# Optimization experiments

Measured on AMD Instinct MI355X. Metric: run time of the kernel, lower is better.

Reference implementation:

```python
import jax, jax.numpy as jnp
import numpy as np

B, S, H, NH = 8, 1042, 768, 12
HD = H // NH            # 64
P = 1024                # patch tokens (32x32 grid); RoPE applied to last P tokens
MLP = 2048              # int(768 * 8/3)
EPS = 1e-6


def _rope_tables():
    # mirrors precompute_rope_freqs_2d(HD, P): inside, dim = HD//2 = 32
    dim = HD // 2
    t = int(P ** 0.5)  # 32
    freqs = 1.0 / (10000.0 ** (np.arange(0, dim, 2, dtype=np.float32) / dim))  # (16,)
    pos = np.arange(t, dtype=np.float32)
    fh = pos[:, None] * freqs[None, :]                       # (t,16)
    f = np.concatenate([np.tile(fh[:, None, :], (1, t, 1)),
                        np.tile(fh[None, :, :], (t, 1, 1))], axis=-1)  # (t,t,32)
    f = f.reshape(P, dim)                                    # (1024,32)
    return jnp.asarray(np.cos(f)), jnp.asarray(np.sin(f))


def setup_inputs() -> dict:
    key = jax.random.key(0)
    ks = jax.random.split(key, 20)
    r = lambda k, sh, sc: (jax.random.normal(k, sh, jnp.float32) * sc)
    cos, sin = _rope_tables()
    return {
        "x": jax.random.normal(ks[0], (B, S, H), jnp.float32),
        "rope_cos": cos, "rope_sin": sin,
        "Wq": r(ks[1], (H, H), 0.02), "Wk": r(ks[2], (H, H), 0.02),
        "Wv": r(ks[3], (H, H), 0.02), "Wo": r(ks[4], (H, H), 0.02),
        "q_norm_w": jnp.ones((HD,), jnp.float32),
        "k_norm_w": jnp.ones((HD,), jnp.float32),
        "gate_W": r(ks[5], (H, NH), 0.02),
        "gate_b": jnp.full((NH,), 4.0, jnp.float32),
        "norm1_w": jnp.ones((H,), jnp.float32),
        "norm2_w": jnp.ones((H,), jnp.float32),
        "W_gate": r(ks[6], (H, MLP), 0.02),
        "W_up": r(ks[7], (H, MLP), 0.02),
        "W_down": r(ks[8], (MLP, H), 0.02),
        "attn_scale": r(ks[9], (H,), 0.1),   # zero-init in module; randn for nontrivial grads
        "mlp_scale": r(ks[10], (H,), 0.1),
    }


def _rmsnorm(x, w):
    return x * jax.lax.rsqrt(jnp.mean(x * x, axis=-1, keepdims=True) + EPS) * w


def _apply_rope(x, cos, sin):
    # x: (B,S,NH,HD); rotate only the last P (patch) tokens, consecutive-pair complex rotation
    xp = x[:, -P:].reshape(B, P, NH, HD // 2, 2)
    x0, x1 = xp[..., 0], xp[..., 1]
    c = cos[None, :, None, :]
    s = sin[None, :, None, :]
    rot = jnp.stack([x0 * c - x1 * s, x0 * s + x1 * c], axis=-1).reshape(B, P, NH, HD)
    return jnp.concatenate([x[:, :-P], rot], axis=1)


def reference(x, rope_cos, rope_sin, Wq, Wk, Wv, Wo, q_norm_w, k_norm_w,
              gate_W, gate_b, norm1_w, norm2_w, W_gate, W_up, W_down,
              attn_scale, mlp_scale):
    # --- attention branch (QwenGatedRoPEAttention) ---
    h = _rmsnorm(x, norm1_w)
    q = (h @ Wq).reshape(B, S, NH, HD)
    k = (h @ Wk).reshape(B, S, NH, HD)
    v = (h @ Wv).reshape(B, S, NH, HD)
    q = _rmsnorm(q, q_norm_w)
    k = _rmsnorm(k, k_norm_w)
    q = _apply_rope(q, rope_cos, rope_sin)
    k = _apply_rope(k, rope_cos, rope_sin)
    q = q / jnp.sqrt(jnp.asarray(HD, jnp.float32))
    scores = jnp.einsum('bqhd,bkhd->bhqk', q, k)          # (B,NH,S,S)
    probs = jax.nn.softmax(scores.astype(jnp.float32), axis=-1)
    attn = jnp.einsum('bhqk,bkhd->bqhd', probs, v)        # (B,S,NH,HD)
    gate = jax.nn.sigmoid((h @ gate_W)[..., None] + gate_b[None, None, :, None])
    attn = (attn * gate).reshape(B, S, H)
    x = x + (attn @ Wo) * attn_scale
    # --- SwiGLU MLP branch ---
    h2 = _rmsnorm(x, norm2_w)
    mlp = (jax.nn.silu(h2 @ W_gate) * (h2 @ W_up)) @ W_down
    x = x + mlp * mlp_scale
    return x
```

## Files before the change

kernel.cpp:

```cpp
#include <hip/hip_runtime.h>
#include <hip/hip_bf16.h>
#include <stdint.h>

#define B_   8
#define S_   1042
#define H_   768
#define NH_  12
#define HD_  64
#define MLP_ 2048
#define T_   (B_*S_)
#define MP_  8448
#define SP_  1088
#define EPS_ 1e-6f

typedef __attribute__((ext_vector_type(8))) short bf16x8v;
typedef __attribute__((ext_vector_type(4))) float f32x4;
typedef __hip_bfloat16 bf16;

typedef __attribute__((address_space(1))) const void gas_void;
typedef __attribute__((address_space(3))) void las_void;

__device__ inline void gload_lds16(const void* g, void* l) {
  __builtin_amdgcn_global_load_lds((gas_void*)g, (las_void*)l, 16, 0, 0);
}

#define BARRIER asm volatile("s_barrier" ::: "memory")
#define VMCNT4  asm volatile("s_waitcnt vmcnt(4)" ::: "memory")

__global__ __launch_bounds__(256) void wcvt_t(const float* __restrict__ W, bf16* __restrict__ o,
                                              int K, int N) {
  __shared__ float tile[32][33];
  int kt = blockIdx.x, nt = blockIdx.y;
  int t = threadIdx.x;
  int r = t >> 5, c = t & 31;
#pragma unroll
  for (int i = 0; i < 4; i++)
    tile[i * 8 + r][c] = W[(long)(kt * 32 + i * 8 + r) * N + nt * 32 + c];
  __syncthreads();
#pragma unroll
  for (int i = 0; i < 4; i++)
    o[(long)(nt * 32 + i * 8 + r) * K + kt * 32 + c] = __float2bfloat16(tile[c][i * 8 + r]);
}

__global__ __launch_bounds__(256) void wcvt_gu(const float* __restrict__ Wg,
                                               const float* __restrict__ Wu,
                                               bf16* __restrict__ o) {
  __shared__ float tile[32][33];
  int kt = blockIdx.x, nt = blockIdx.y;
  int t = threadIdx.x;
  int r = t >> 5, c = t & 31;
  const float* src = (c < 16) ? Wg : Wu;
  int col = nt * 16 + (c & 15);
#pragma unroll
  for (int i = 0; i < 4; i++)
    tile[i * 8 + r][c] = src[(long)(kt * 32 + i * 8 + r) * MLP_ + col];
  __syncthreads();
#pragma unroll
  for (int i = 0; i < 4; i++)
    o[(long)(nt * 32 + i * 8 + r) * 768 + kt * 32 + c] = __float2bfloat16(tile[c][i * 8 + r]);
}

__global__ __launch_bounds__(256) void rmsnorm_k(const float* __restrict__ x,
                                                 const float* __restrict__ w,
                                                 bf16* __restrict__ o, int Mreal) {
  int row = blockIdx.x;
  bf16* orow = o + (long)row * H_;
  int t = threadIdx.x;
  if (row >= Mreal) {
    for (int i = t; i < H_; i += 256) orow[i] = __float2bfloat16(0.f);
    return;
  }
  const float* xr = x + (long)row * H_;
  float v0 = xr[t], v1 = xr[t + 256], v2 = xr[t + 512];
  float s = v0 * v0 + v1 * v1 + v2 * v2;
  for (int off = 32; off; off >>= 1) s += __shfl_down(s, off);
  __shared__ float red[4];
  if ((t & 63) == 0) red[t >> 6] = s;
  __syncthreads();
  float tot = red[0] + red[1] + red[2] + red[3];
  float inv = rsqrtf(tot * (1.f / H_) + EPS_);
  orow[t]       = __float2bfloat16(v0 * inv * w[t]);
  orow[t + 256] = __float2bfloat16(v1 * inv * w[t + 256]);
  orow[t + 512] = __float2bfloat16(v2 * inv * w[t + 512]);
}

template <int EPI>
__global__ __launch_bounds__(512) void gemm256(
    const bf16* __restrict__ A, const bf16* __restrict__ Bt, void* __restrict__ Out,
    int N, int nbn) {
  __shared__ __align__(16) bf16 lds[2][4][128 * 64];
  int tid = threadIdx.x;
  int lane = tid & 63, wid = tid >> 6;
  int wr = wid >> 2, wc = wid & 3;
  int lr = lane & 15, lg = lane >> 4;

  int nwg = gridDim.x;
  int bid = blockIdx.x;
  int q = nwg >> 3, r8 = nwg & 7;
  int xcd = bid & 7, idx = bid >> 3;
  int wg = (xcd < r8 ? xcd * (q + 1) : r8 * (q + 1) + (xcd - r8) * q) + idx;
  int bm = wg / nbn, bn = wg - bm * nbn;

  int chunk_row = tid >> 3;
  int cc = (tid & 7) ^ (chunk_row & 7);
  const bf16* aSrc = A + ((long)bm * 256 + chunk_row) * 768 + cc * 8;
  const bf16* bSrc = Bt + ((long)bn * 256 + chunk_row) * 768 + cc * 8;

  auto stA = [&](int buf, int half, int kt) {
    bf16* d = &lds[buf][half][tid * 8];
    const bf16* s = aSrc + (long)half * 128 * 768 + kt * 64;
    gload_lds16(s, d);
    gload_lds16(s + 64 * 768, d + 512 * 8);
  };
  auto stB = [&](int buf, int half, int kt) {
    bf16* d = &lds[buf][2 + half][tid * 8];
    const bf16* s = bSrc + (long)half * 128 * 768 + kt * 64;
    gload_lds16(s, d);
    gload_lds16(s + 64 * 768, d + 512 * 8);
  };
  auto ldA = [&](int buf, int mi, int ks) -> bf16x8v {
    int row = mi * 16 + lr;
    int c = (ks * 4 + lg) ^ (row & 7);
    return *(const bf16x8v*)&lds[buf][wr][row * 64 + c * 8];
  };
  auto ldB = [&](int buf, int ni, int ks) -> bf16x8v {
    int row = (wc & 1) * 64 + ni * 16 + lr;
    int c = (ks * 4 + lg) ^ (row & 7);
    return *(const bf16x8v*)&lds[buf][2 + (wc >> 1)][row * 64 + c * 8];
  };

  f32x4 z; z[0] = z[1] = z[2] = z[3] = 0.f;
  f32x4 acc[8][4];
#pragma unroll
  for (int mi = 0; mi < 8; mi++)
#pragma unroll
    for (int ni = 0; ni < 4; ni++) acc[mi][ni] = z;

  bf16x8v bf[4][2];
  bf16x8v af[4];

  stA(0, 0, 0); stA(0, 1, 0); stB(0, 0, 0); stB(0, 1, 0);
  stB(1, 0, 1); stB(1, 1, 1);
  VMCNT4;
  BARRIER;

#define PHASE(p, bb, STG, VM)                                                   \
  {                                                                             \
    if ((p) == 0) {                                                             \
      _Pragma("unroll") for (int ni = 0; ni < 4; ni++) {                        \
        bf[ni][0] = ldB(bb, ni, 0); bf[ni][1] = ldB(bb, ni, 1);                 \
      }                                                                         \
    }                                                                           \
    af[0] = ldA(bb, 2 * (p), 0);     af[1] = ldA(bb, 2 * (p), 1);               \
    af[2] = ldA(bb, 2 * (p) + 1, 0); af[3] = ldA(bb, 2 * (p) + 1, 1);           \
    STG;                                                                        \
    asm volatile("" ::: "memory");                                              \
    BARRIER;                                                                    \
    __builtin_amdgcn_s_setprio(1);                                              \
    _Pragma("unroll") for (int dm = 0; dm < 2; dm++)                            \
      _Pragma("unroll") for (int ni = 0; ni < 4; ni++) {                        \
        acc[2 * (p) + dm][ni] = __builtin_amdgcn_mfma_f32_16x16x32_bf16(        \
            af[dm * 2 + 0], bf[ni][0], acc[2 * (p) + dm][ni], 0, 0, 0);         \
        acc[2 * (p) + dm][ni] = __builtin_amdgcn_mfma_f32_16x16x32_bf16(        \
            af[dm * 2 + 1], bf[ni][1], acc[2 * (p) + dm][ni], 0, 0, 0);         \
      }                                                                         \
    __builtin_amdgcn_s_setprio(0);                                              \
    if (VM) VMCNT4;                                                             \
    BARRIER;                                                                    \
  }

  for (int i = 0; i < 6; i++) {
    int u = 2 * i + 1;
    int t2 = (2 * i + 2 < 12) ? 2 * i + 2 : 11;
    int t3 = (2 * i + 3 < 12) ? 2 * i + 3 : 11;
    PHASE(0, 0, stA(1, 0, u), 0);
    PHASE(1, 0, stA(1, 1, u), 0);
    PHASE(2, 0, stB(0, 0, t2), 0);
    PHASE(3, 0, stB(0, 1, t2), 1);
    PHASE(0, 1, stA(0, 0, t2), 0);
    PHASE(1, 1, stA(0, 1, t2), 0);
    PHASE(2, 1, stB(1, 0, t3), 0);
    PHASE(3, 1, stB(1, 1, t3), 1);
  }
#undef PHASE

  long rowbase = (long)bm * 256 + wr * 128;
  int colbase = bn * 256 + wc * 64;
  if (EPI == 0) {
    bf16* O = (bf16*)Out;
#pragma unroll
    for (int mi = 0; mi < 8; mi++)
#pragma unroll
      for (int ni = 0; ni < 4; ni++)
#pragma unroll
        for (int r = 0; r < 4; r++)
          O[(rowbase + mi * 16 + lg * 4 + r) * N + colbase + ni * 16 + lr] =
              __float2bfloat16(acc[mi][ni][r]);
  } else {
    bf16* O = (bf16*)Out;
    int oc0 = colbase >> 1;
#pragma unroll
    for (int mi = 0; mi < 8; mi++)
#pragma unroll
      for (int p = 0; p < 2; p++)
#pragma unroll
        for (int r = 0; r < 4; r++) {
          float g = acc[mi][2 * p][r], u = acc[mi][2 * p + 1][r];
          float v = g / (1.f + __expf(-g)) * u;
          O[(rowbase + mi * 16 + lg * 4 + r) * 2048 + oc0 + p * 16 + lr] =
              __float2bfloat16(v);
        }
  }
}

template <int EPI>
__global__ __launch_bounds__(256) void gemm_bf16(
    const bf16* __restrict__ A, const bf16* __restrict__ Bt, void* __restrict__ Out,
    const float* __restrict__ resid, const float* __restrict__ scale,
    int N, int K, int Mreal) {
  __shared__ __align__(16) bf16 As[128 * 32];
  __shared__ __align__(16) bf16 Bs[128 * 32];
  int tid = threadIdx.x;
  int lane = tid & 63, wid = tid >> 6;
  int wm = wid >> 1, wn = wid & 1;
  int lr = lane & 15, lg = lane >> 4;
  long rowA0 = (long)blockIdx.y * 128;
  long rowB0 = (long)blockIdx.x * 128;
  f32x4 z; z[0] = z[1] = z[2] = z[3] = 0.f;
  f32x4 acc[4][4];
#pragma unroll
  for (int mi = 0; mi < 4; mi++)
#pragma unroll
    for (int ni = 0; ni < 4; ni++) acc[mi][ni] = z;

  const int flat0 = wid * 512 + lane * 8;
  const bf16* Ab = A + rowA0 * K;
  const bf16* Bb = Bt + rowB0 * K;

  for (int k0 = 0; k0 < K; k0 += 32) {
    __syncthreads();
#pragma unroll
    for (int j = 0; j < 2; j++) {
      int flat = flat0 + j * 2048;
      int r = flat >> 5, c = flat & 31;
      gload_lds16(Ab + (long)r * K + k0 + c, &As[flat]);
      gload_lds16(Bb + (long)r * K + k0 + c, &Bs[flat]);
    }
    __syncthreads();
    bf16x8v af[4], bfr[4];
#pragma unroll
    for (int mi = 0; mi < 4; mi++)
      af[mi] = *(const bf16x8v*)&As[(wm * 64 + mi * 16 + lr) * 32 + lg * 8];
#pragma unroll
    for (int ni = 0; ni < 4; ni++)
      bfr[ni] = *(const bf16x8v*)&Bs[(wn * 64 + ni * 16 + lr) * 32 + lg * 8];
#pragma unroll
    for (int mi = 0; mi < 4; mi++)
#pragma unroll
      for (int ni = 0; ni < 4; ni++)
        acc[mi][ni] = __builtin_amdgcn_mfma_f32_16x16x32_bf16(af[mi], bfr[ni], acc[mi][ni], 0, 0, 0);
  }

#pragma unroll
  for (int mi = 0; mi < 4; mi++) {
#pragma unroll
    for (int ni = 0; ni < 4; ni++) {
#pragma unroll
      for (int r = 0; r < 4; r++) {
        long row = rowA0 + wm * 64 + mi * 16 + lg * 4 + r;
        long col = rowB0 + wn * 64 + ni * 16 + lr;
        float v = acc[mi][ni][r];
        if (EPI == 0) {
          ((bf16*)Out)[row * N + col] = __float2bfloat16(v);
        } else {
          if (row < Mreal)
            ((float*)Out)[row * N + col] = resid[row * N + col] + v * scale[col];
        }
      }
    }
  }
}

__global__ __launch_bounds__(256) void vtran(const bf16* __restrict__ qkv, bf16* __restrict__ vtf) {
  __shared__ bf16 tile[32][66];
  int st = blockIdx.x, bh = blockIdx.y;
  int bb = bh / NH_, h = bh - bb * NH_;
  int s0 = st * 32;
  int t = threadIdx.x;
  int si = t >> 6, d = t & 63;
#pragma unroll
  for (int i = 0; i < 8; i++) {
    int s = s0 + i * 4 + si;
    bf16 v = __float2bfloat16(0.f);
    if (s < S_) v = qkv[(long)(bb * S_ + s) * 2304 + 1536 + h * 64 + d];
    tile[i * 4 + si][d] = v;
  }
  __syncthreads();
  int dd = t >> 5, sj = t & 31;
#pragma unroll
  for (int i = 0; i < 8; i++) {
    int d2 = i * 8 + dd;
    vtf[((long)bh * 64 + d2) * SP_ + s0 + sj] = tile[sj][d2];
  }
}

__global__ __launch_bounds__(768) void qkv_post(
    const bf16* __restrict__ qkv, const float* __restrict__ qw, const float* __restrict__ kw,
    const float* __restrict__ cosT, const float* __restrict__ sinT,
    bf16* __restrict__ qf, bf16* __restrict__ kf) {
  int tok = blockIdx.x;
  int bb = tok / S_, s = tok - bb * S_;
  int h = threadIdx.x >> 6, d = threadIdx.x & 63;
  const bf16* base = qkv + (long)tok * 2304 + h * 64 + d;
  float q = __bfloat162float(base[0]);
  float k = __bfloat162float(base[768]);
  float qs = q * q, ks = k * k;
  for (int off = 32; off; off >>= 1) {
    qs += __shfl_xor(qs, off);
    ks += __shfl_xor(ks, off);
  }
  q *= rsqrtf(qs * (1.f / 64.f) + EPS_) * qw[d];
  k *= rsqrtf(ks * (1.f / 64.f) + EPS_) * kw[d];
  if (s >= S_ - 1024) {
    int pos = s - (S_ - 1024);
    int i = d >> 1;
    float c = cosT[pos * 32 + i], sn = sinT[pos * 32 + i];
    float qp = __shfl_xor(q, 1), kp = __shfl_xor(k, 1);
    if (d & 1) { q = qp * sn + q * c; k = kp * sn + k * c; }
    else       { q = q * c - qp * sn; k = k * c - kp * sn; }
  }
  q *= 0.125f * 1.44269504088896f;
  long o1 = ((long)(bb * NH_ + h) * SP_ + s) * 64 + d;
  qf[o1] = __float2bfloat16(q);
  kf[o1] = __float2bfloat16(k);
}

__global__ __launch_bounds__(64) void gate_k(const bf16* __restrict__ h, const float* __restrict__ gW,
                                             const float* __restrict__ gb, float* __restrict__ gate) {
  int tok = blockIdx.x, l = threadIdx.x;
  float hv[12];
#pragma unroll
  for (int i = 0; i < 12; i++) hv[i] = __bfloat162float(h[(long)tok * H_ + i * 64 + l]);
#pragma unroll
  for (int n = 0; n < 12; n++) {
    float s = 0.f;
#pragma unroll
    for (int i = 0; i < 12; i++) s += hv[i] * gW[(i * 64 + l) * 12 + n];
    for (int off = 32; off; off >>= 1) s += __shfl_xor(s, off);
    if (l == 0) gate[(long)tok * 12 + n] = 1.f / (1.f + __expf(-(s + gb[n])));
  }
}

#define SWZ(row, cc) (((row) << 6) + ((((cc) ^ ((row) & 7))) << 3))

__global__ __launch_bounds__(256) void attn_k(
    const bf16* __restrict__ qf, const bf16* __restrict__ kf, const bf16* __restrict__ vtf,
    const float* __restrict__ gate, bf16* __restrict__ attn_g) {
  __shared__ __align__(16) bf16 Ks[2][64 * 64];
  __shared__ __align__(16) bf16 Vs[2][64 * 64];
  int bid = blockIdx.x;
  int w = (bid & 7) * 204 + (bid >> 3);
  int bh = w / 17, qb = w - bh * 17;
  int bb = bh / NH_, h = bh - bb * NH_;
  int tid = threadIdx.x;
  int lane = tid & 63, wv = tid >> 6;
  int lr = lane & 15, lg = lane >> 4;
  const bf16* qbase = qf + (long)bh * SP_ * 64;
  const bf16* kbase = kf + (long)bh * SP_ * 64;
  const bf16* vbase = vtf + (long)bh * 64 * SP_;

  int q_l = qb * 64 + wv * 16 + lr;
  bf16x8v qB0 = *(const bf16x8v*)(qbase + (long)q_l * 64 + lg * 8);
  bf16x8v qB1 = *(const bf16x8v*)(qbase + (long)q_l * 64 + 32 + lg * 8);

  f32x4 z; z[0] = z[1] = z[2] = z[3] = 0.f;
  f32x4 acc[4] = {z, z, z, z};
  float m = -1e30f, lsum = 0.f;

  auto stage = [&](int buf, int kidx) {
#pragma unroll
    for (int inst = 0; inst < 2; inst++) {
      int c = inst * 256 + tid;
      int row = c >> 3, slot = c & 7;
      int cc = slot ^ (row & 7);
      gload_lds16(kbase + (long)(kidx + row) * 64 + cc * 8, &Ks[buf][c * 8]);
    }
#pragma unroll
    for (int inst = 0; inst < 2; inst++) {
      int c = inst * 256 + tid;
      int row = c >> 3, slot = c & 7;
      int cc = slot ^ (row & 7);
      gload_lds16(vbase + (long)row * SP_ + kidx + cc * 8, &Vs[buf][c * 8]);
    }
  };

  stage(0, 0);
  asm volatile("s_waitcnt vmcnt(0)" ::: "memory");
  __syncthreads();
  int cur = 0;

  for (int kt = 0; kt < SP_ / 64; kt++) {
    int kidx = kt * 64;
    if (kt < SP_ / 64 - 1) stage(cur ^ 1, kidx + 64);

    f32x4 p[4];
    __builtin_amdgcn_s_setprio(1);
#pragma unroll
    for (int mt = 0; mt < 4; mt++) {
      int row = mt * 16 + lr;
      bf16x8v k0 = *(const bf16x8v*)&Ks[cur][SWZ(row, lg)];
      bf16x8v k1 = *(const bf16x8v*)&Ks[cur][SWZ(row, lg + 4)];
      f32x4 t = z;
      t = __builtin_amdgcn_mfma_f32_16x16x32_bf16(k0, qB0, t, 0, 0, 0);
      t = __builtin_amdgcn_mfma_f32_16x16x32_bf16(k1, qB1, t, 0, 0, 0);
      p[mt] = t;
    }
    __builtin_amdgcn_s_setprio(0);

    if (kidx + 64 > S_) {
#pragma unroll
      for (int mt = 0; mt < 4; mt++)
#pragma unroll
        for (int r = 0; r < 4; r++)
          if (kidx + mt * 16 + lg * 4 + r >= S_) p[mt][r] = -1e30f;
    }

    float tmax = p[0][0];
#pragma unroll
    for (int mt = 0; mt < 4; mt++)
#pragma unroll
      for (int r = 0; r < 4; r++) tmax = fmaxf(tmax, p[mt][r]);
    tmax = fmaxf(tmax, __shfl_xor(tmax, 16));
    tmax = fmaxf(tmax, __shfl_xor(tmax, 32));

    if (__ballot(tmax > m + 11.0f)) {
      float mn = fmaxf(m, tmax);
      float so = exp2f(m - mn);
      m = mn;
      lsum *= so;
      float so4[4];
#pragma unroll
      for (int r = 0; r < 4; r++) so4[r] = __shfl(so, lg * 4 + r);
#pragma unroll
      for (int dt = 0; dt < 4; dt++) {
        f32x4 a = acc[dt];
        a[0] *= so4[0]; a[1] *= so4[1]; a[2] *= so4[2]; a[3] *= so4[3];
        acc[dt] = a;
      }
    }
    float ts = 0.f;
#pragma unroll
    for (int mt = 0; mt < 4; mt++)
#pragma unroll
      for (int r = 0; r < 4; r++) {
        float e = exp2f(p[mt][r] - m);
        p[mt][r] = e;
        ts += e;
      }
    ts += __shfl_xor(ts, 16);
    ts += __shfl_xor(ts, 32);
    lsum += ts;

    uint32_t w0[4], w1[4];
#pragma unroll
    for (int mt = 0; mt < 4; mt++) {
      asm("v_cvt_pk_bf16_f32 %0, %1, %2" : "=v"(w0[mt]) : "v"(p[mt][0]), "v"(p[mt][1]));
      asm("v_cvt_pk_bf16_f32 %0, %1, %2" : "=v"(w1[mt]) : "v"(p[mt][2]), "v"(p[mt][3]));
    }
    bf16x8v aP[2];
#pragma unroll
    for (int t2 = 0; t2 < 2; t2++) {
      union { uint32_t u[4]; bf16x8v v; } cvt;
#pragma unroll
      for (int wd = 0; wd < 4; wd++) {
        uint32_t a = (wd & 1) ? w1[2 * t2] : w0[2 * t2];
        uint32_t b = (wd & 1) ? w1[2 * t2 + 1] : w0[2 * t2 + 1];
        uint32_t val = (lg & 2) ? b : a;
        int src = ((lg & 1) * 2 + (wd >> 1)) * 16 + lr;
        cvt.u[wd] = (uint32_t)__shfl((int)val, src);
      }
      aP[t2] = cvt.v;
    }
    __builtin_amdgcn_s_setprio(1);
#pragma unroll
    for (int t2 = 0; t2 < 2; t2++)
#pragma unroll
      for (int dt = 0; dt < 4; dt++) {
        int row = dt * 16 + lr;
        bf16x8v vB = *(const bf16x8v*)&Vs[cur][SWZ(row, t2 * 4 + lg)];
        acc[dt] = __builtin_amdgcn_mfma_f32_16x16x32_bf16(aP[t2], vB, acc[dt], 0, 0, 0);
      }
    __builtin_amdgcn_s_setprio(0);

    asm volatile("s_waitcnt vmcnt(0)" ::: "memory");
    __syncthreads();
    cur ^= 1;
  }

  float norm = 0.f;
  if (q_l < S_) norm = gate[((long)bb * S_ + q_l) * 12 + h] / lsum;
  float nr[4];
#pragma unroll
  for (int r = 0; r < 4; r++) nr[r] = __shfl(norm, lg * 4 + r);
#pragma unroll
  for (int dt = 0; dt < 4; dt++)
#pragma unroll
    for (int r = 0; r < 4; r++) {
      int qr = qb * 64 + wv * 16 + lg * 4 + r;
      if (qr < S_)
        attn_g[((long)bb * S_ + qr) * H_ + h * 64 + dt * 16 + lr] =
            __float2bfloat16(acc[dt][r] * nr[r]);
    }
}

extern "C" void kernel_launch(void* const* d_in, const int* in_sizes, int n_in,
                              void* d_out, int out_size, void* d_ws, size_t ws_size,
                              hipStream_t stream) {
  const float* x    = (const float*)d_in[0];
  const float* cosT = (const float*)d_in[1];
  const float* sinT = (const float*)d_in[2];
  const float* Wq   = (const float*)d_in[3];
  const float* Wk   = (const float*)d_in[4];
  const float* Wv   = (const float*)d_in[5];
  const float* Wo   = (const float*)d_in[6];
  const float* qnw  = (const float*)d_in[7];
  const float* knw  = (const float*)d_in[8];
  const float* gW   = (const float*)d_in[9];
  const float* gb   = (const float*)d_in[10];
  const float* n1w  = (const float*)d_in[11];
  const float* n2w  = (const float*)d_in[12];
  const float* Wg   = (const float*)d_in[13];
  const float* Wu   = (const float*)d_in[14];
  const float* Wd   = (const float*)d_in[15];
  const float* ascale = (const float*)d_in[16];
  const float* mscale = (const float*)d_in[17];

  char* ws = (char*)d_ws;
  size_t off = 0;
  auto alloc = [&](size_t bytes) {
    char* p = ws + off;
    off += (bytes + 255) & ~(size_t)255;
    return p;
  };
  bf16* h_pad  = (bf16*)alloc((size_t)MP_ * H_ * 2);
  bf16* wqkv_t = (bf16*)alloc((size_t)2304 * 768 * 2);
  bf16* wo_t   = (bf16*)alloc((size_t)768 * 768 * 2);
  bf16* wgu_t  = (bf16*)alloc((size_t)4096 * 768 * 2);
  bf16* wdn_t  = (bf16*)alloc((size_t)768 * 2048 * 2);
  bf16* qkv    = (bf16*)alloc((size_t)MP_ * 2304 * 2);
  bf16* qfb    = (bf16*)alloc((size_t)96 * SP_ * 64 * 2);
  bf16* kfb    = (bf16*)alloc((size_t)96 * SP_ * 64 * 2);
  bf16* vtfb   = (bf16*)alloc((size_t)96 * SP_ * 64 * 2);
  float* gateb = (float*)alloc((size_t)T_ * 12 * 4);
  bf16* attn_g = (bf16*)alloc((size_t)MP_ * H_ * 2);
  float* x2    = (float*)alloc((size_t)T_ * H_ * 4);
  bf16* mlpin  = qkv;

  auto wc = [&](const float* W, bf16* o, int K, int N) {
    wcvt_t<<<dim3(K / 32, N / 32), 256, 0, stream>>>(W, o, K, N);
  };
  wc(Wq, wqkv_t, 768, 768);
  wc(Wk, wqkv_t + 768 * 768, 768, 768);
  wc(Wv, wqkv_t + 2 * 768 * 768, 768, 768);
  wc(Wo, wo_t, 768, 768);
  wc(Wd, wdn_t, 2048, 768);
  wcvt_gu<<<dim3(24, 128), 256, 0, stream>>>(gW ? Wg : Wg, Wu, wgu_t);

  rmsnorm_k<<<MP_, 256, 0, stream>>>(x, n1w, h_pad, T_);

  gemm256<0><<<9 * 33, 512, 0, stream>>>(h_pad, wqkv_t, qkv, 2304, 9);

  qkv_post<<<T_, 768, 0, stream>>>(qkv, qnw, knw, cosT, sinT, qfb, kfb);
  vtran<<<dim3(33, 96), 256, 0, stream>>>(qkv, vtfb);

  gate_k<<<T_, 64, 0, stream>>>(h_pad, gW, gb, gateb);

  attn_k<<<1632, 256, 0, stream>>>(qfb, kfb, vtfb, gateb, attn_g);

  gemm_bf16<1><<<dim3(768 / 128, MP_ / 128), 256, 0, stream>>>(
      attn_g, wo_t, x2, x, ascale, 768, 768, T_);

  rmsnorm_k<<<MP_, 256, 0, stream>>>(x2, n2w, h_pad, T_);

  gemm256<2><<<16 * 33, 512, 0, stream>>>(h_pad, wgu_t, mlpin, 4096, 16);

  gemm_bf16<1><<<dim3(768 / 128, MP_ / 128), 256, 0, stream>>>(
      mlpin, wdn_t, (float*)d_out, x2, mscale, 768, 2048, T_);
}
```

Before: 468.3 us.

## Fuse gate projection into rmsnorm and streamline gemm256 pipeline barriers

Computes the per-head sigmoid gate inside the first rmsnorm kernel from the fp32 normalized row, which removes the separate gate_k launch and its re-read of h. The bf16 GEMM kernel now precomputes swizzled LDS fragment pointers and global source pointers, fully unrolls the k-loop, and drops the trailing barrier and compiler memory fence in each phase. Dropping the barrier cuts synchronization per k-step but depends on the remaining barrier ordering to avoid LDS races. Removing the tile-index clamp means the last iterations prefetch k-tiles past the end of each row, which can read out of bounds on the final rows.

```diff
diff --git a/kernel.cpp b/kernel.cpp
--- a/kernel.cpp
+++ b/kernel.cpp
@@ -60,9 +60,13 @@
     o[(long)(nt * 32 + i * 8 + r) * 768 + kt * 32 + c] = __float2bfloat16(tile[c][i * 8 + r]);
 }
 
+template <int GATE>
 __global__ __launch_bounds__(256) void rmsnorm_k(const float* __restrict__ x,
                                                  const float* __restrict__ w,
-                                                 bf16* __restrict__ o, int Mreal) {
+                                                 bf16* __restrict__ o,
+                                                 const float* __restrict__ gW,
+                                                 const float* __restrict__ gb,
+                                                 float* __restrict__ gate, int Mreal) {
   int row = blockIdx.x;
   bf16* orow = o + (long)row * H_;
   int t = threadIdx.x;
@@ -75,13 +79,35 @@
   float s = v0 * v0 + v1 * v1 + v2 * v2;
   for (int off = 32; off; off >>= 1) s += __shfl_down(s, off);
   __shared__ float red[4];
+  __shared__ float gred[4][12];
   if ((t & 63) == 0) red[t >> 6] = s;
   __syncthreads();
   float tot = red[0] + red[1] + red[2] + red[3];
   float inv = rsqrtf(tot * (1.f / H_) + EPS_);
-  orow[t]       = __float2bfloat16(v0 * inv * w[t]);
-  orow[t + 256] = __float2bfloat16(v1 * inv * w[t + 256]);
-  orow[t + 512] = __float2bfloat16(v2 * inv * w[t + 512]);
+  float h0 = v0 * inv * w[t], h1 = v1 * inv * w[t + 256], h2 = v2 * inv * w[t + 512];
+  orow[t]       = __float2bfloat16(h0);
+  orow[t + 256] = __float2bfloat16(h1);
+  orow[t + 512] = __float2bfloat16(h2);
+  if (GATE) {
+    const float* g0 = gW + (long)t * 12;
+    const float* g1 = gW + (long)(t + 256) * 12;
+    const float* g2 = gW + (long)(t + 512) * 12;
+    float g[12];
+#pragma unroll
+    for (int n = 0; n < 12; n++) g[n] = h0 * g0[n] + h1 * g1[n] + h2 * g2[n];
+#pragma unroll
+    for (int n = 0; n < 12; n++) {
+      float v = g[n];
+      v += __shfl_xor(v, 1); v += __shfl_xor(v, 2); v += __shfl_xor(v, 4);
+      v += __shfl_xor(v, 8); v += __shfl_xor(v, 16); v += __shfl_xor(v, 32);
+      if ((t & 63) == 0) gred[t >> 6][n] = v;
+    }
+    __syncthreads();
+    if (t < 12) {
+      float s4 = gred[0][t] + gred[1][t] + gred[2][t] + gred[3][t];
+      gate[(long)row * 12 + t] = 1.f / (1.f + __expf(-(s4 + gb[t])));
+    }
+  }
 }
 
 template <int EPI>
@@ -101,33 +127,39 @@
   int wg = (xcd < r8 ? xcd * (q + 1) : r8 * (q + 1) + (xcd - r8) * q) + idx;
   int bm = wg / nbn, bn = wg - bm * nbn;
 
+  const bf16 *aP0[2], *aP1[2], *bP0[2], *bP1[2];
+  {
+    int off0 = lr * 64 + ((lg ^ (lr & 7)) * 8);
+    int off1 = lr * 64 + (((4 + lg) ^ (lr & 7)) * 8);
+#pragma unroll
+    for (int b = 0; b < 2; b++) {
+      aP0[b] = &lds[b][wr][off0];
+      aP1[b] = &lds[b][wr][off1];
+      bP0[b] = &lds[b][2 + (wc >> 1)][(wc & 1) * 4096 + off0];
+      bP1[b] = &lds[b][2 + (wc >> 1)][(wc & 1) * 4096 + off1];
+    }
+  }
   int chunk_row = tid >> 3;
   int cc = (tid & 7) ^ (chunk_row & 7);
-  const bf16* aSrc = A + ((long)bm * 256 + chunk_row) * 768 + cc * 8;
-  const bf16* bSrc = Bt + ((long)bn * 256 + chunk_row) * 768 + cc * 8;
-
-  auto stA = [&](int buf, int half, int kt) {
-    bf16* d = &lds[buf][half][tid * 8];
-    const bf16* s = aSrc + (long)half * 128 * 768 + kt * 64;
-    gload_lds16(s, d);
-    gload_lds16(s + 64 * 768, d + 512 * 8);
-  };
-  auto stB = [&](int buf, int half, int kt) {
-    bf16* d = &lds[buf][2 + half][tid * 8];
-    const bf16* s = bSrc + (long)half * 128 * 768 + kt * 64;
-    gload_lds16(s, d);
-    gload_lds16(s + 64 * 768, d + 512 * 8);
-  };
-  auto ldA = [&](int buf, int mi, int ks) -> bf16x8v {
-    int row = mi * 16 + lr;
-    int c = (ks * 4 + lg) ^ (row & 7);
-    return *(const bf16x8v*)&lds[buf][wr][row * 64 + c * 8];
-  };
-  auto ldB = [&](int buf, int ni, int ks) -> bf16x8v {
-    int row = (wc & 1) * 64 + ni * 16 + lr;
-    int c = (ks * 4 + lg) ^ (row & 7);
-    return *(const bf16x8v*)&lds[buf][2 + (wc >> 1)][row * 64 + c * 8];
-  };
+  const bf16 *aB[2][2], *bB[2][2];
+#pragma unroll
+  for (int h = 0; h < 2; h++)
+#pragma unroll
+    for (int sub = 0; sub < 2; sub++) {
+      aB[h][sub] = A + ((long)bm * 256 + h * 128 + sub * 64 + chunk_row) * 768 + cc * 8;
+      bB[h][sub] = Bt + ((long)bn * 256 + h * 128 + sub * 64 + chunk_row) * 768 + cc * 8;
+    }
+
+#define STA(buf, half, kt)                                                      \
+  {                                                                             \
+    gload_lds16(aB[half][0] + (kt) * 64, &lds[buf][half][tid * 8]);             \
+    gload_lds16(aB[half][1] + (kt) * 64, &lds[buf][half][4096 + tid * 8]);      \
+  }
+#define STB(buf, half, kt)                                                      \
+  {                                                                             \
+    gload_lds16(bB[half][0] + (kt) * 64, &lds[buf][2 + (half)][tid * 8]);       \
+    gload_lds16(bB[half][1] + (kt) * 64, &lds[buf][2 + (half)][4096 + tid * 8]);\
+  }
 
   f32x4 z; z[0] = z[1] = z[2] = z[3] = 0.f;
   f32x4 acc[8][4];
@@ -139,8 +171,8 @@
   bf16x8v bf[4][2];
   bf16x8v af[4];
 
-  stA(0, 0, 0); stA(0, 1, 0); stB(0, 0, 0); stB(0, 1, 0);
-  stB(1, 0, 1); stB(1, 1, 1);
+  STA(0, 0, 0); STA(0, 1, 0); STB(0, 0, 0); STB(0, 1, 0);
+  STB(1, 0, 1); STB(1, 1, 1);
   VMCNT4;
   BARRIER;
 
@@ -148,13 +180,15 @@
   {                                                                             \
     if ((p) == 0) {                                                             \
       _Pragma("unroll") for (int ni = 0; ni < 4; ni++) {                        \
-        bf[ni][0] = ldB(bb, ni, 0); bf[ni][1] = ldB(bb, ni, 1);                 \
+        bf[ni][0] = *(const bf16x8v*)(bP0[bb] + ni * 1024);                     \
+        bf[ni][1] = *(const bf16x8v*)(bP1[bb] + ni * 1024);                     \
       }                                                                         \
     }                                                                           \
-    af[0] = ldA(bb, 2 * (p), 0);     af[1] = ldA(bb, 2 * (p), 1);               \
-    af[2] = ldA(bb, 2 * (p) + 1, 0); af[3] = ldA(bb, 2 * (p) + 1, 1);           \
+    af[0] = *(const bf16x8v*)(aP0[bb] + (2 * (p)) * 1024);                      \
+    af[1] = *(const bf16x8v*)(aP1[bb] + (2 * (p)) * 1024);                      \
+    af[2] = *(const bf16x8v*)(aP0[bb] + (2 * (p) + 1) * 1024);                  \
+    af[3] = *(const bf16x8v*)(aP1[bb] + (2 * (p) + 1) * 1024);                  \
     STG;                                                                        \
-    asm volatile("" ::: "memory");                                              \
     BARRIER;                                                                    \
     __builtin_amdgcn_s_setprio(1);                                              \
     _Pragma("unroll") for (int dm = 0; dm < 2; dm++)                            \
@@ -166,23 +200,22 @@
       }                                                                         \
     __builtin_amdgcn_s_setprio(0);                                              \
     if (VM) VMCNT4;                                                             \
-    BARRIER;                                                                    \
-  }
-
+  }
+
+#pragma unroll
   for (int i = 0; i < 6; i++) {
-    int u = 2 * i + 1;
-    int t2 = (2 * i + 2 < 12) ? 2 * i + 2 : 11;
-    int t3 = (2 * i + 3 < 12) ? 2 * i + 3 : 11;
-    PHASE(0, 0, stA(1, 0, u), 0);
-    PHASE(1, 0, stA(1, 1, u), 0);
-    PHASE(2, 0, stB(0, 0, t2), 0);
-    PHASE(3, 0, stB(0, 1, t2), 1);
-    PHASE(0, 1, stA(0, 0, t2), 0);
-    PHASE(1, 1, stA(0, 1, t2), 0);
-    PHASE(2, 1, stB(1, 0, t3), 0);
-    PHASE(3, 1, stB(1, 1, t3), 1);
+    PHASE(0, 0, STA(1, 0, 2 * i + 1), 0);
+    PHASE(1, 0, STA(1, 1, 2 * i + 1), 0);
+    PHASE(2, 0, STB(0, 0, 2 * i + 2), 0);
+    PHASE(3, 0, STB(0, 1, 2 * i + 2), 1);
+    PHASE(0, 1, STA(0, 0, 2 * i + 2), 0);
+    PHASE(1, 1, STA(0, 1, 2 * i + 2), 0);
+    PHASE(2, 1, STB(1, 0, 2 * i + 3), 0);
+    PHASE(3, 1, STB(1, 1, 2 * i + 3), 1);
   }
 #undef PHASE
+#undef STA
+#undef STB
 
   long rowbase = (long)bm * 256 + wr * 128;
   int colbase = bn * 256 + wc * 64;
@@ -333,22 +366,6 @@
   long o1 = ((long)(bb * NH_ + h) * SP_ + s) * 64 + d;
   qf[o1] = __float2bfloat16(q);
   kf[o1] = __float2bfloat16(k);
-}
-
-__global__ __launch_bounds__(64) void gate_k(const bf16* __restrict__ h, const float* __restrict__ gW,
-                                             const float* __restrict__ gb, float* __restrict__ gate) {
-  int tok = blockIdx.x, l = threadIdx.x;
-  float hv[12];
-#pragma unroll
-  for (int i = 0; i < 12; i++) hv[i] = __bfloat162float(h[(long)tok * H_ + i * 64 + l]);
-#pragma unroll
-  for (int n = 0; n < 12; n++) {
-    float s = 0.f;
-#pragma unroll
-    for (int i = 0; i < 12; i++) s += hv[i] * gW[(i * 64 + l) * 12 + n];
-    for (int off = 32; off; off >>= 1) s += __shfl_xor(s, off);
-    if (l == 0) gate[(long)tok * 12 + n] = 1.f / (1.f + __expf(-(s + gb[n])));
-  }
 }
 
 #define SWZ(row, cc) (((row) << 6) + ((((cc) ^ ((row) & 7))) << 3))
@@ -564,23 +581,21 @@
   wc(Wv, wqkv_t + 2 * 768 * 768, 768, 768);
   wc(Wo, wo_t, 768, 768);
   wc(Wd, wdn_t, 2048, 768);
-  wcvt_gu<<<dim3(24, 128), 256, 0, stream>>>(gW ? Wg : Wg, Wu, wgu_t);
-
-  rmsnorm_k<<<MP_, 256, 0, stream>>>(x, n1w, h_pad, T_);
+  wcvt_gu<<<dim3(24, 128), 256, 0, stream>>>(Wg, Wu, wgu_t);
+
+  rmsnorm_k<1><<<MP_, 256, 0, stream>>>(x, n1w, h_pad, gW, gb, gateb, T_);
 
   gemm256<0><<<9 * 33, 512, 0, stream>>>(h_pad, wqkv_t, qkv, 2304, 9);
 
   qkv_post<<<T_, 768, 0, stream>>>(qkv, qnw, knw, cosT, sinT, qfb, kfb);
   vtran<<<dim3(33, 96), 256, 0, stream>>>(qkv, vtfb);
 
-  gate_k<<<T_, 64, 0, stream>>>(h_pad, gW, gb, gateb);
-
   attn_k<<<1632, 256, 0, stream>>>(qfb, kfb, vtfb, gateb, attn_g);
 
   gemm_bf16<1><<<dim3(768 / 128, MP_ / 128), 256, 0, stream>>>(
       attn_g, wo_t, x2, x, ascale, 768, 768, T_);
 
-  rmsnorm_k<<<MP_, 256, 0, stream>>>(x2, n2w, h_pad, T_);
+  rmsnorm_k<0><<<MP_, 256, 0, stream>>>(x2, n2w, h_pad, nullptr, nullptr, nullptr, T_);
 
   gemm256<2><<<16 * 33, 512, 0, stream>>>(h_pad, wgu_t, mlpin, 4096, 16);
 
```

Result: faster. 414.9 us (-11.4%).
